# Kernel optimization log

Hardware: AMD Instinct MI355X
Metric: run time of the kernel (lower is better)

The kernel has to match this reference:

```python
import jax, jax.numpy as jnp
import numpy as np

N_NODES = 100000
N_EDGES = 1600000
N_FEAT = 128
N_HID = 128
N_CLS = 40
DROP_P = 0.5


def setup_inputs() -> dict:
    key = jax.random.key(0)
    k1, k2, k3, k4 = jax.random.split(key, 4)
    x = jax.random.normal(k1, (N_NODES, N_FEAT), dtype=jnp.float32)
    edge_index = jax.random.randint(k2, (2, N_EDGES), 0, N_NODES, dtype=jnp.int32)
    W1 = jax.random.normal(k3, (N_FEAT, N_HID), dtype=jnp.float32) / np.sqrt(N_FEAT)
    b1 = jnp.zeros((N_HID,), dtype=jnp.float32)
    W2 = jax.random.normal(k4, (N_HID, N_CLS), dtype=jnp.float32) / np.sqrt(N_HID)
    b2 = jnp.zeros((N_CLS,), dtype=jnp.float32)
    return {"x": x, "edge_index": edge_index, "W1": W1, "b1": b1, "W2": W2, "b2": b2}


def _gcn_norm(edge_index, num_nodes):
    # add self-loops, then symmetric normalization D^-1/2 (A+I) D^-1/2
    loops = jnp.arange(num_nodes, dtype=edge_index.dtype)
    src = jnp.concatenate([edge_index[0], loops])
    dst = jnp.concatenate([edge_index[1], loops])
    deg = jax.ops.segment_sum(jnp.ones_like(dst, dtype=jnp.float32), dst,
                              num_segments=num_nodes)
    deg_isqrt = jax.lax.rsqrt(deg)  # deg >= 1 thanks to self-loops
    norm = deg_isqrt[src] * deg_isqrt[dst]  # [E+N]
    return src, dst, norm


def _gcn_conv(x, src, dst, norm, W, b, num_nodes):
    h = x @ W                                   # [N, out]
    msg = h[src] * norm[:, None]                # gather + scale, [E+N, out]
    out = jax.ops.segment_sum(msg, dst, num_segments=num_nodes)  # scatter-add
    return out + b


def reference(x, edge_index, W1, b1, W2, b2):
    num_nodes = x.shape[0]
    src, dst, norm = _gcn_norm(edge_index, num_nodes)
    h = _gcn_conv(x, src, dst, norm, W1, b1, num_nodes)
    h = jax.nn.relu(h)
    # dropout(p=0.5, training=True) with a fixed key for determinism
    keep = jax.random.uniform(jax.random.key(42), h.shape) >= DROP_P
    h = jnp.where(keep, h / (1.0 - DROP_P), 0.0)
    out = _gcn_conv(h, src, dst, norm, W2, b2, num_nodes)
    return out
```

## Files before the change

### kernel.cpp

```cpp
#include <hip/hip_runtime.h>

#define N_NODES 100000
#define N_EDGES 1600000
#define NBUCK 196
#define G1B 1563
#define FB 391
#define FEDGE 4096
#define BCAP 9216

typedef __attribute__((ext_vector_type(8))) short short8v;
typedef __attribute__((ext_vector_type(4))) float f32x4;

__device__ __forceinline__ unsigned pack_bf16(float a, float b){
  unsigned ua = __float_as_uint(a), ub = __float_as_uint(b);
  ua = ua + 0x7fffu + ((ua >> 16) & 1u);
  ub = ub + 0x7fffu + ((ub >> 16) & 1u);
  return (ua >> 16) | (ub & 0xffff0000u);
}
__device__ __forceinline__ unsigned short bf16_of(float a){
  unsigned ua = __float_as_uint(a);
  ua = ua + 0x7fffu + ((ua >> 16) & 1u);
  return (unsigned short)(ua >> 16);
}
__device__ __forceinline__ float bf_lo(unsigned u){ return __uint_as_float(u << 16); }
__device__ __forceinline__ float bf_hi(unsigned u){ return __uint_as_float(u & 0xffff0000u); }

__device__ __forceinline__ unsigned tf_rotl(unsigned x, int r){ return (x<<r)|(x>>(32-r)); }

__device__ __forceinline__ unsigned dropout_keep(unsigned e){
  unsigned x0 = 0u, x1 = e;
  const unsigned k0 = 0u, k1v = 42u;
  const unsigned k2 = 0x1BD11BDAu ^ k0 ^ k1v;
#define TF_R(r) { x0 += x1; x1 = tf_rotl(x1,(r)); x1 ^= x0; }
  x0 += k0; x1 += k1v;
  TF_R(13) TF_R(15) TF_R(26) TF_R(6)
  x0 += k1v; x1 += k2 + 1u;
  TF_R(17) TF_R(29) TF_R(16) TF_R(24)
  x0 += k2; x1 += k0 + 2u;
  TF_R(13) TF_R(15) TF_R(26) TF_R(6)
  x0 += k0; x1 += k1v + 3u;
  TF_R(17) TF_R(29) TF_R(16) TF_R(24)
  x0 += k1v; x1 += k2 + 4u;
  TF_R(13) TF_R(15) TF_R(26) TF_R(6)
  x0 += k2; x1 += k0 + 5u;
#undef TF_R
  return (x0 ^ x1) >> 31;
}

__global__ void k_wt(const float* __restrict__ W1, unsigned short* __restrict__ W1T){
  int idx = blockIdx.x*256 + threadIdx.x;
  int k = idx >> 7, n = idx & 127;
  W1T[n*128 + k] = bf16_of(W1[idx]);
}

__launch_bounds__(256)
__global__ void k_B(const float* __restrict__ x, const unsigned short* __restrict__ W1T,
                    unsigned short* __restrict__ h1u,
                    const int* __restrict__ src, const int* __restrict__ dst,
                    int* __restrict__ bcur2, int2* __restrict__ tmp, int N, int E){
  __shared__ int hist[NBUCK];
  int t = threadIdx.x;
  if (blockIdx.x < FB){
    int fb = blockIdx.x;
    for (int i = t; i < NBUCK; i += 256) hist[i] = 0;
    __syncthreads();
    int e0 = fb*FEDGE;
    #pragma unroll 4
    for (int j = 0; j < FEDGE/256; j++){
      int e = e0 + t + j*256;
      if (e < E) atomicAdd(&hist[dst[e] >> 9], 1);
    }
    __syncthreads();
    if (t < NBUCK){
      int c = hist[t];
      if (c > 0) hist[t] = t*BCAP + atomicAdd(&bcur2[t], c);
    }
    __syncthreads();
    #pragma unroll 4
    for (int j = 0; j < FEDGE/256; j++){
      int e = e0 + t + j*256;
      if (e < E){
        int d = dst[e], s = src[e];
        int p = atomicAdd(&hist[d >> 9], 1);
        tmp[p] = make_int2(s, d);
      }
    }
    return;
  }
  int gb = blockIdx.x - FB;
  if (gb >= G1B) return;
  int w = t >> 6, l = t & 63;
  int lo = l & 15, hi = l >> 4;
  int rowA = gb*64 + w*16 + lo;
  int rA = (rowA < N) ? rowA : (N-1);
  const float4* xr = (const float4*)(x + (size_t)rA*128);

  short8v a[4];
  #pragma unroll
  for (int kk = 0; kk < 4; kk++){
    float4 f0 = xr[kk*8 + 2*hi];
    float4 f1 = xr[kk*8 + 2*hi + 1];
    union { short8v v; unsigned u[4]; } A;
    A.u[0] = pack_bf16(f0.x, f0.y);
    A.u[1] = pack_bf16(f0.z, f0.w);
    A.u[2] = pack_bf16(f1.x, f1.y);
    A.u[3] = pack_bf16(f1.z, f1.w);
    a[kk] = A.v;
  }
  int rowC0 = gb*64 + w*16 + hi*4;
  #pragma unroll
  for (int tt = 0; tt < 8; tt++){
    int n0 = tt*16;
    const uint4* brow = (const uint4*)(W1T + (n0 + lo)*128);
    f32x4 acc = {0.f, 0.f, 0.f, 0.f};
    #pragma unroll
    for (int kk = 0; kk < 4; kk++){
      union { short8v v; uint4 q; } B;
      B.q = brow[kk*4 + hi];
      acc = __builtin_amdgcn_mfma_f32_16x16x32_bf16(a[kk], B.v, acc, 0, 0, 0);
    }
    int colC = n0 + lo;
    #pragma unroll
    for (int r = 0; r < 4; r++){
      int rc = rowC0 + r;
      if (rc < N) h1u[(size_t)rc*128 + colC] = bf16_of(acc[r]);
    }
  }
}

__launch_bounds__(512)
__global__ void k_hist(const int2* __restrict__ tmp, const int* __restrict__ bcur2,
                       int* __restrict__ degi, int* __restrict__ off,
                       float* __restrict__ dii, int N){
  __shared__ int cur[512];
  __shared__ int wtot[8];
  int b = blockIdx.x, t = threadIdx.x;
  cur[t] = 0;
  __syncthreads();
  int m = bcur2[b];
  int base = b*BCAP;
  int node0 = b << 9;
  for (int i = t; i < m; i += 512)
    atomicAdd(&cur[tmp[base + i].y - node0], 1);
  __syncthreads();
  int v = cur[t];
  int lane = t & 63, w = t >> 6;
  int incl = v;
  for (int d = 1; d < 64; d <<= 1){
    int y = __shfl_up(incl, d);
    if (lane >= d) incl += y;
  }
  if (lane == 63) wtot[w] = incl;
  __syncthreads();
  int wb = 0;
  for (int i = 0; i < w; i++) wb += wtot[i];
  int excl = wb + incl - v;
  int n = node0 + t;
  if (n < N){
    degi[n] = v;
    off[n]  = base + excl;
    dii[n]  = rsqrtf((float)(v + 1));
  }
}

__launch_bounds__(1024)
__global__ void k_csort(const int2* __restrict__ tmp, int2* __restrict__ csre,
                        const int* __restrict__ off, const int* __restrict__ bcur2,
                        const float* __restrict__ dii, int N){
  __shared__ int   cur[512];
  __shared__ float dl[512];
  int b = blockIdx.x, t = threadIdx.x;
  int node0 = b << 9;
  if (t < 512){
    int n = node0 + t;
    cur[t] = (n < N) ? off[n] : 0;
    dl[t]  = (n < N) ? dii[n] : 0.f;
  }
  __syncthreads();
  int m = bcur2[b];
  int base = b*BCAP;
  for (int i = t; i < m; i += 1024){
    int2 r = tmp[base + i];
    int dloc = r.y - node0;
    float w = dii[r.x] * dl[dloc];
    int p = atomicAdd(&cur[dloc], 1);
    csre[p] = make_int2(r.x, __float_as_int(w));
  }
}

__launch_bounds__(256)
__global__ void k_agg1(const unsigned* __restrict__ h1g, unsigned* __restrict__ Bbg,
                       const int2* __restrict__ csre, const int* __restrict__ off,
                       const int* __restrict__ degi, const float* __restrict__ dii,
                       const float* __restrict__ b1, int N){
  int n = blockIdx.x*4 + (threadIdx.x >> 6);
  int lane = threadIdx.x & 63;
  if (n >= N) return;
  n = __builtin_amdgcn_readfirstlane(n);
  float din = dii[n];
  float s2 = din*din;
  unsigned su = h1g[(size_t)n*64 + lane];
  float a0 = bf_lo(su)*s2, a1 = bf_hi(su)*s2;
  int o = off[n], cnt = degi[n];
  int i = 0;
  for (; i + 8 <= cnt; i += 8){
    int2 e0 = csre[o+i+0], e1 = csre[o+i+1], e2 = csre[o+i+2], e3 = csre[o+i+3];
    int2 e4 = csre[o+i+4], e5 = csre[o+i+5], e6 = csre[o+i+6], e7 = csre[o+i+7];
    unsigned u0 = h1g[(size_t)e0.x*64 + lane];
    unsigned u1 = h1g[(size_t)e1.x*64 + lane];
    unsigned u2 = h1g[(size_t)e2.x*64 + lane];
    unsigned u3 = h1g[(size_t)e3.x*64 + lane];
    unsigned u4 = h1g[(size_t)e4.x*64 + lane];
    unsigned u5 = h1g[(size_t)e5.x*64 + lane];
    unsigned u6 = h1g[(size_t)e6.x*64 + lane];
    unsigned u7 = h1g[(size_t)e7.x*64 + lane];
    float w0 = __int_as_float(e0.y), w1 = __int_as_float(e1.y);
    float w2 = __int_as_float(e2.y), w3 = __int_as_float(e3.y);
    float w4 = __int_as_float(e4.y), w5 = __int_as_float(e5.y);
    float w6 = __int_as_float(e6.y), w7 = __int_as_float(e7.y);
    a0 = fmaf(bf_lo(u0), w0, a0); a1 = fmaf(bf_hi(u0), w0, a1);
    a0 = fmaf(bf_lo(u1), w1, a0); a1 = fmaf(bf_hi(u1), w1, a1);
    a0 = fmaf(bf_lo(u2), w2, a0); a1 = fmaf(bf_hi(u2), w2, a1);
    a0 = fmaf(bf_lo(u3), w3, a0); a1 = fmaf(bf_hi(u3), w3, a1);
    a0 = fmaf(bf_lo(u4), w4, a0); a1 = fmaf(bf_hi(u4), w4, a1);
    a0 = fmaf(bf_lo(u5), w5, a0); a1 = fmaf(bf_hi(u5), w5, a1);
    a0 = fmaf(bf_lo(u6), w6, a0); a1 = fmaf(bf_hi(u6), w6, a1);
    a0 = fmaf(bf_lo(u7), w7, a0); a1 = fmaf(bf_hi(u7), w7, a1);
  }
  for (; i < cnt; ++i){
    int2 e = csre[o+i];
    unsigned u = h1g[(size_t)e.x*64 + lane];
    float w = __int_as_float(e.y);
    a0 = fmaf(bf_lo(u), w, a0); a1 = fmaf(bf_hi(u), w, a1);
  }
  float2 bb = *(const float2*)(b1 + lane*2);
  a0 = fmaxf(a0 + bb.x, 0.f);
  a1 = fmaxf(a1 + bb.y, 0.f);
  unsigned e0i = (unsigned)n*128u + (unsigned)lane*2u;
  a0 = dropout_keep(e0i)      ? a0*2.f : 0.f;
  a1 = dropout_keep(e0i + 1u) ? a1*2.f : 0.f;
  Bbg[(size_t)n*64 + lane] = pack_bf16(a0, a1);
}

__launch_bounds__(256)
__global__ void k_gemm2(const unsigned* __restrict__ Bbg, const float* __restrict__ W2,
                        unsigned short* __restrict__ h2p, int N){
  __shared__ float W2T[40*132];
  __shared__ float Bs[64*132];
  int t = threadIdx.x;
  int row0 = blockIdx.x * 64;
  for (int idx = t; idx < 128*40; idx += 256){
    int r = idx / 40, c = idx - 40*r;
    W2T[c*132 + r] = W2[idx];
  }
  #pragma unroll
  for (int j = 0; j < 8; j++){
    int idx = t + 256*j;
    int r = idx >> 5, c2 = idx & 31;
    int gr = row0 + r; if (gr > N-1) gr = N-1;
    uint2 v = *(const uint2*)(Bbg + (size_t)gr*64 + c2*2);
    float4 f = { bf_lo(v.x), bf_hi(v.x), bf_lo(v.y), bf_hi(v.y) };
    *(float4*)(Bs + r*132 + c2*4) = f;
  }
  __syncthreads();

  int cg = t & 7, rg = t >> 3;
  int c0 = cg*5, r0 = rg*2;
  float acc[2][5] = {};
  #pragma unroll 4
  for (int k = 0; k < 128; k++){
    float bv0 = Bs[r0*132 + k], bv1 = Bs[(r0+1)*132 + k];
    #pragma unroll
    for (int u = 0; u < 5; u++){
      float w = W2T[(c0+u)*132 + k];
      acc[0][u] = fmaf(bv0, w, acc[0][u]);
      acc[1][u] = fmaf(bv1, w, acc[1][u]);
    }
  }
  #pragma unroll
  for (int i = 0; i < 2; i++){
    int gr = row0 + r0 + i;
    if (gr < N){
      #pragma unroll
      for (int u = 0; u < 5; u++) h2p[(size_t)gr*64 + c0 + u] = bf16_of(acc[i][u]);
    }
  }
}

__launch_bounds__(256)
__global__ void k_agg2(const unsigned* __restrict__ h2p, float* __restrict__ out,
                       const int2* __restrict__ csre, const int* __restrict__ off,
                       const int* __restrict__ degi, const float* __restrict__ dii,
                       const float* __restrict__ b2, int N){
  int n = blockIdx.x*4 + (threadIdx.x >> 6);
  int lane31 = threadIdx.x & 31;
  int lane   = threadIdx.x & 63;
  if (n >= N) return;
  n = __builtin_amdgcn_readfirstlane(n);
  float din = dii[n];
  float s2 = din*din;
  unsigned su = h2p[(size_t)n*32 + lane31];
  float a0 = bf_lo(su)*s2, a1 = bf_hi(su)*s2;
  int o = off[n], cnt = degi[n];
  int i = 0;
  for (; i + 8 <= cnt; i += 8){
    int2 e0 = csre[o+i+0], e1 = csre[o+i+1], e2 = csre[o+i+2], e3 = csre[o+i+3];
    int2 e4 = csre[o+i+4], e5 = csre[o+i+5], e6 = csre[o+i+6], e7 = csre[o+i+7];
    unsigned u0 = h2p[(size_t)e0.x*32 + lane31];
    unsigned u1 = h2p[(size_t)e1.x*32 + lane31];
    unsigned u2 = h2p[(size_t)e2.x*32 + lane31];
    unsigned u3 = h2p[(size_t)e3.x*32 + lane31];
    unsigned u4 = h2p[(size_t)e4.x*32 + lane31];
    unsigned u5 = h2p[(size_t)e5.x*32 + lane31];
    unsigned u6 = h2p[(size_t)e6.x*32 + lane31];
    unsigned u7 = h2p[(size_t)e7.x*32 + lane31];
    float w0 = __int_as_float(e0.y), w1 = __int_as_float(e1.y);
    float w2 = __int_as_float(e2.y), w3 = __int_as_float(e3.y);
    float w4 = __int_as_float(e4.y), w5 = __int_as_float(e5.y);
    float w6 = __int_as_float(e6.y), w7 = __int_as_float(e7.y);
    a0 = fmaf(bf_lo(u0), w0, a0); a1 = fmaf(bf_hi(u0), w0, a1);
    a0 = fmaf(bf_lo(u1), w1, a0); a1 = fmaf(bf_hi(u1), w1, a1);
    a0 = fmaf(bf_lo(u2), w2, a0); a1 = fmaf(bf_hi(u2), w2, a1);
    a0 = fmaf(bf_lo(u3), w3, a0); a1 = fmaf(bf_hi(u3), w3, a1);
    a0 = fmaf(bf_lo(u4), w4, a0); a1 = fmaf(bf_hi(u4), w4, a1);
    a0 = fmaf(bf_lo(u5), w5, a0); a1 = fmaf(bf_hi(u5), w5, a1);
    a0 = fmaf(bf_lo(u6), w6, a0); a1 = fmaf(bf_hi(u6), w6, a1);
    a0 = fmaf(bf_lo(u7), w7, a0); a1 = fmaf(bf_hi(u7), w7, a1);
  }
  for (; i < cnt; ++i){
    int2 e = csre[o+i];
    unsigned u = h2p[(size_t)e.x*32 + lane31];
    float w = __int_as_float(e.y);
    a0 = fmaf(bf_lo(u), w, a0); a1 = fmaf(bf_hi(u), w, a1);
  }
  if (lane < 20){
    float2 bb = *(const float2*)(b2 + lane*2);
    a0 += bb.x;
    a1 += bb.y;
    *(float2*)(out + (size_t)n*40 + lane*2) = make_float2(a0, a1);
  }
}

extern "C" void kernel_launch(void* const* d_in, const int* in_sizes, int n_in,
                              void* d_out, int out_size, void* d_ws, size_t ws_size,
                              hipStream_t stream){
  const float* x  = (const float*)d_in[0];
  const int*   ei = (const int*)  d_in[1];
  const float* W1 = (const float*)d_in[2];
  const float* b1 = (const float*)d_in[3];
  const float* W2 = (const float*)d_in[4];
  const float* b2 = (const float*)d_in[5];
  float* out = (float*)d_out;
  char* ws = (char*)d_ws;
  const int N = N_NODES, E = N_EDGES;
  const int* srcv = ei;
  const int* dstv = ei + E;

  int*   bcur2 = (int*)  (ws + 0);
  int*   off   = (int*)  (ws + 8192);
  int*   degi  = (int*)  (ws + 417792);
  float* dii   = (float*)(ws + 827392);
  unsigned short* W1T = (unsigned short*)(ws + 1236992);
  int2*  tmp   = (int2*) (ws + 1269760);
  int2*  csre  = (int2*) (ws + 15720448);
  unsigned short* h1u = (unsigned short*)(ws + 30171136);
  unsigned*       h1g = (unsigned*)      (ws + 30171136);
  unsigned short* h2p = (unsigned short*)(ws + 30171136);
  unsigned*       Bbg = (unsigned*)      (ws + 55771136);

  hipMemsetAsync(bcur2, 0, 8192, stream);
  k_wt<<<64, 256, 0, stream>>>(W1, W1T);

  k_B<<<FB + G1B, 256, 0, stream>>>(x, W1T, h1u, srcv, dstv, bcur2, tmp, N, E);
  k_hist<<<NBUCK, 512, 0, stream>>>(tmp, bcur2, degi, off, dii, N);
  k_csort<<<NBUCK, 1024, 0, stream>>>(tmp, csre, off, bcur2, dii, N);

  k_agg1 <<<N/4, 256, 0, stream>>>(h1g, Bbg, csre, off, degi, dii, b1, N);
  k_gemm2<<<(N + 63)/64, 256, 0, stream>>>(Bbg, W2, h2p, N);
  k_agg2 <<<N/4, 256, 0, stream>>>((const unsigned*)h2p, out, csre, off, degi, dii, b2, N);
}
```

Before: 229.7 us.

## Pack edges to 32 bits, merge sort kernels, use MFMA for second GEMM

Packs src and local dst into one 32-bit word and stores only the source index in the CSR, recomputing normalization weights from dii during aggregation. Merges the histogram and counting-sort kernels into one, folds the memset and weight transposes into a single init kernel, and replaces the scalar LDS-based second GEMM with bf16 MFMA using a padded transposed W2. This reduces edge-list bandwidth and launch count, at the cost of an extra dii gather per edge in both aggregation kernels.

```diff
diff --git a/kernel.cpp b/kernel.cpp
--- a/kernel.cpp
+++ b/kernel.cpp
@@ -47,17 +47,28 @@
   return (x0 ^ x1) >> 31;
 }
 
-__global__ void k_wt(const float* __restrict__ W1, unsigned short* __restrict__ W1T){
-  int idx = blockIdx.x*256 + threadIdx.x;
-  int k = idx >> 7, n = idx & 127;
-  W1T[n*128 + k] = bf16_of(W1[idx]);
+__global__ void k_init(const float* __restrict__ W1, const float* __restrict__ W2,
+                       unsigned short* __restrict__ W1T, unsigned short* __restrict__ W2T48,
+                       int* __restrict__ bcur2){
+  int b = blockIdx.x, t = threadIdx.x;
+  if (b < 64){
+    int idx = b*256 + t;
+    int k = idx >> 7, n = idx & 127;
+    W1T[n*128 + k] = bf16_of(W1[idx]);
+  } else {
+    if (t < NBUCK) bcur2[t] = 0;
+    for (int i = t; i < 48*128; i += 256){
+      int c = i >> 7, k = i & 127;
+      W2T48[c*128 + k] = (c < 40) ? bf16_of(W2[k*40 + c]) : (unsigned short)0;
+    }
+  }
 }
 
 __launch_bounds__(256)
 __global__ void k_B(const float* __restrict__ x, const unsigned short* __restrict__ W1T,
                     unsigned short* __restrict__ h1u,
                     const int* __restrict__ src, const int* __restrict__ dst,
-                    int* __restrict__ bcur2, int2* __restrict__ tmp, int N, int E){
+                    int* __restrict__ bcur2, unsigned* __restrict__ tmp, int N, int E){
   __shared__ int hist[NBUCK];
   int t = threadIdx.x;
   if (blockIdx.x < FB){
@@ -82,7 +93,7 @@
       if (e < E){
         int d = dst[e], s = src[e];
         int p = atomicAdd(&hist[d >> 9], 1);
-        tmp[p] = make_int2(s, d);
+        tmp[p] = ((unsigned)(d & 511) << 17) | (unsigned)s;
       }
     }
     return;
@@ -128,69 +139,58 @@
   }
 }
 
-__launch_bounds__(512)
-__global__ void k_hist(const int2* __restrict__ tmp, const int* __restrict__ bcur2,
+__launch_bounds__(1024)
+__global__ void k_sort(const unsigned* __restrict__ tmp, const int* __restrict__ bcur2,
                        int* __restrict__ degi, int* __restrict__ off,
-                       float* __restrict__ dii, int N){
+                       float* __restrict__ dii, unsigned* __restrict__ csr, int N){
   __shared__ int cur[512];
   __shared__ int wtot[8];
   int b = blockIdx.x, t = threadIdx.x;
-  cur[t] = 0;
+  if (t < 512) cur[t] = 0;
   __syncthreads();
   int m = bcur2[b];
   int base = b*BCAP;
   int node0 = b << 9;
-  for (int i = t; i < m; i += 512)
-    atomicAdd(&cur[tmp[base + i].y - node0], 1);
+  for (int i = t; i < m; i += 1024)
+    atomicAdd(&cur[tmp[base + i] >> 17], 1);
   __syncthreads();
-  int v = cur[t];
-  int lane = t & 63, w = t >> 6;
-  int incl = v;
-  for (int d = 1; d < 64; d <<= 1){
-    int y = __shfl_up(incl, d);
-    if (lane >= d) incl += y;
-  }
-  if (lane == 63) wtot[w] = incl;
+  int v = 0, excl = 0;
+  if (t < 512){
+    v = cur[t];
+    int lane = t & 63, w = t >> 6;
+    int incl = v;
+    for (int d = 1; d < 64; d <<= 1){
+      int y = __shfl_up(incl, d);
+      if (lane >= d) incl += y;
+    }
+    if (lane == 63) wtot[w] = incl;
+    __syncthreads();
+    int wb = 0;
+    for (int i = 0; i < w; i++) wb += wtot[i];
+    excl = wb + incl - v;
+    int n = node0 + t;
+    if (n < N){
+      degi[n] = v;
+      off[n]  = base + excl;
+      dii[n]  = rsqrtf((float)(v + 1));
+    }
+  } else {
+    __syncthreads();
+  }
   __syncthreads();
-  int wb = 0;
-  for (int i = 0; i < w; i++) wb += wtot[i];
-  int excl = wb + incl - v;
-  int n = node0 + t;
-  if (n < N){
-    degi[n] = v;
-    off[n]  = base + excl;
-    dii[n]  = rsqrtf((float)(v + 1));
-  }
-}
-
-__launch_bounds__(1024)
-__global__ void k_csort(const int2* __restrict__ tmp, int2* __restrict__ csre,
-                        const int* __restrict__ off, const int* __restrict__ bcur2,
-                        const float* __restrict__ dii, int N){
-  __shared__ int   cur[512];
-  __shared__ float dl[512];
-  int b = blockIdx.x, t = threadIdx.x;
-  int node0 = b << 9;
-  if (t < 512){
-    int n = node0 + t;
-    cur[t] = (n < N) ? off[n] : 0;
-    dl[t]  = (n < N) ? dii[n] : 0.f;
-  }
+  if (t < 512) cur[t] = base + excl;
   __syncthreads();
-  int m = bcur2[b];
-  int base = b*BCAP;
   for (int i = t; i < m; i += 1024){
-    int2 r = tmp[base + i];
-    int dloc = r.y - node0;
-    float w = dii[r.x] * dl[dloc];
+    unsigned e = tmp[base + i];
+    int dloc = e >> 17;
     int p = atomicAdd(&cur[dloc], 1);
-    csre[p] = make_int2(r.x, __float_as_int(w));
+    csr[p] = e & 0x1FFFFu;
   }
 }
 
 __launch_bounds__(256)
 __global__ void k_agg1(const unsigned* __restrict__ h1g, unsigned* __restrict__ Bbg,
-                       const int2* __restrict__ csre, const int* __restrict__ off,
+                       const unsigned* __restrict__ csr, const int* __restrict__ off,
                        const int* __restrict__ degi, const float* __restrict__ dii,
                        const float* __restrict__ b1, int N){
   int n = blockIdx.x*4 + (threadIdx.x >> 6);
@@ -204,20 +204,18 @@
   int o = off[n], cnt = degi[n];
   int i = 0;
   for (; i + 8 <= cnt; i += 8){
-    int2 e0 = csre[o+i+0], e1 = csre[o+i+1], e2 = csre[o+i+2], e3 = csre[o+i+3];
-    int2 e4 = csre[o+i+4], e5 = csre[o+i+5], e6 = csre[o+i+6], e7 = csre[o+i+7];
-    unsigned u0 = h1g[(size_t)e0.x*64 + lane];
-    unsigned u1 = h1g[(size_t)e1.x*64 + lane];
-    unsigned u2 = h1g[(size_t)e2.x*64 + lane];
-    unsigned u3 = h1g[(size_t)e3.x*64 + lane];
-    unsigned u4 = h1g[(size_t)e4.x*64 + lane];
-    unsigned u5 = h1g[(size_t)e5.x*64 + lane];
-    unsigned u6 = h1g[(size_t)e6.x*64 + lane];
-    unsigned u7 = h1g[(size_t)e7.x*64 + lane];
-    float w0 = __int_as_float(e0.y), w1 = __int_as_float(e1.y);
-    float w2 = __int_as_float(e2.y), w3 = __int_as_float(e3.y);
-    float w4 = __int_as_float(e4.y), w5 = __int_as_float(e5.y);
-    float w6 = __int_as_float(e6.y), w7 = __int_as_float(e7.y);
+    unsigned s0 = csr[o+i+0], s1 = csr[o+i+1], s2i = csr[o+i+2], s3 = csr[o+i+3];
+    unsigned s4 = csr[o+i+4], s5 = csr[o+i+5], s6 = csr[o+i+6], s7 = csr[o+i+7];
+    float w0 = dii[s0]*din, w1 = dii[s1]*din, w2 = dii[s2i]*din, w3 = dii[s3]*din;
+    float w4 = dii[s4]*din, w5 = dii[s5]*din, w6 = dii[s6]*din, w7 = dii[s7]*din;
+    unsigned u0 = h1g[(size_t)s0*64 + lane];
+    unsigned u1 = h1g[(size_t)s1*64 + lane];
+    unsigned u2 = h1g[(size_t)s2i*64 + lane];
+    unsigned u3 = h1g[(size_t)s3*64 + lane];
+    unsigned u4 = h1g[(size_t)s4*64 + lane];
+    unsigned u5 = h1g[(size_t)s5*64 + lane];
+    unsigned u6 = h1g[(size_t)s6*64 + lane];
+    unsigned u7 = h1g[(size_t)s7*64 + lane];
     a0 = fmaf(bf_lo(u0), w0, a0); a1 = fmaf(bf_hi(u0), w0, a1);
     a0 = fmaf(bf_lo(u1), w1, a0); a1 = fmaf(bf_hi(u1), w1, a1);
     a0 = fmaf(bf_lo(u2), w2, a0); a1 = fmaf(bf_hi(u2), w2, a1);
@@ -228,9 +226,9 @@
     a0 = fmaf(bf_lo(u7), w7, a0); a1 = fmaf(bf_hi(u7), w7, a1);
   }
   for (; i < cnt; ++i){
-    int2 e = csre[o+i];
-    unsigned u = h1g[(size_t)e.x*64 + lane];
-    float w = __int_as_float(e.y);
+    unsigned s = csr[o+i];
+    float w = dii[s]*din;
+    unsigned u = h1g[(size_t)s*64 + lane];
     a0 = fmaf(bf_lo(u), w, a0); a1 = fmaf(bf_hi(u), w, a1);
   }
   float2 bb = *(const float2*)(b1 + lane*2);
@@ -243,53 +241,46 @@
 }
 
 __launch_bounds__(256)
-__global__ void k_gemm2(const unsigned* __restrict__ Bbg, const float* __restrict__ W2,
+__global__ void k_gemm2(const unsigned* __restrict__ Bbg, const unsigned short* __restrict__ W2T48,
                         unsigned short* __restrict__ h2p, int N){
-  __shared__ float W2T[40*132];
-  __shared__ float Bs[64*132];
   int t = threadIdx.x;
-  int row0 = blockIdx.x * 64;
-  for (int idx = t; idx < 128*40; idx += 256){
-    int r = idx / 40, c = idx - 40*r;
-    W2T[c*132 + r] = W2[idx];
-  }
+  int w = t >> 6, l = t & 63;
+  int lo = l & 15, hi = l >> 4;
+  int rowA = blockIdx.x*64 + w*16 + lo;
+  int rA = (rowA < N) ? rowA : (N-1);
+  const uint4* ar = (const uint4*)(Bbg + (size_t)rA*64);
+
+  short8v a[4];
   #pragma unroll
-  for (int j = 0; j < 8; j++){
-    int idx = t + 256*j;
-    int r = idx >> 5, c2 = idx & 31;
-    int gr = row0 + r; if (gr > N-1) gr = N-1;
-    uint2 v = *(const uint2*)(Bbg + (size_t)gr*64 + c2*2);
-    float4 f = { bf_lo(v.x), bf_hi(v.x), bf_lo(v.y), bf_hi(v.y) };
-    *(float4*)(Bs + r*132 + c2*4) = f;
-  }
-  __syncthreads();
-
-  int cg = t & 7, rg = t >> 3;
-  int c0 = cg*5, r0 = rg*2;
-  float acc[2][5] = {};
-  #pragma unroll 4
-  for (int k = 0; k < 128; k++){
-    float bv0 = Bs[r0*132 + k], bv1 = Bs[(r0+1)*132 + k];
+  for (int kk = 0; kk < 4; kk++){
+    union { short8v v; uint4 q; } A;
+    A.q = ar[kk*4 + hi];
+    a[kk] = A.v;
+  }
+  int rowC0 = blockIdx.x*64 + w*16 + hi*4;
+  #pragma unroll
+  for (int tt = 0; tt < 3; tt++){
+    int n0 = tt*16;
+    const uint4* brow = (const uint4*)(W2T48 + (n0 + lo)*128);
+    f32x4 acc = {0.f, 0.f, 0.f, 0.f};
     #pragma unroll
-    for (int u = 0; u < 5; u++){
-      float w = W2T[(c0+u)*132 + k];
-      acc[0][u] = fmaf(bv0, w, acc[0][u]);
-      acc[1][u] = fmaf(bv1, w, acc[1][u]);
-    }
-  }
-  #pragma unroll
-  for (int i = 0; i < 2; i++){
-    int gr = row0 + r0 + i;
-    if (gr < N){
-      #pragma unroll
-      for (int u = 0; u < 5; u++) h2p[(size_t)gr*64 + c0 + u] = bf16_of(acc[i][u]);
+    for (int kk = 0; kk < 4; kk++){
+      union { short8v v; uint4 q; } B;
+      B.q = brow[kk*4 + hi];
+      acc = __builtin_amdgcn_mfma_f32_16x16x32_bf16(a[kk], B.v, acc, 0, 0, 0);
+    }
+    int colC = n0 + lo;
+    #pragma unroll
+    for (int r = 0; r < 4; r++){
+      int rc = rowC0 + r;
+      if (rc < N) h2p[(size_t)rc*64 + colC] = bf16_of(acc[r]);
     }
   }
 }
 
 __launch_bounds__(256)
 __global__ void k_agg2(const unsigned* __restrict__ h2p, float* __restrict__ out,
-                       const int2* __restrict__ csre, const int* __restrict__ off,
+                       const unsigned* __restrict__ csr, const int* __restrict__ off,
                        const int* __restrict__ degi, const float* __restrict__ dii,
                        const float* __restrict__ b2, int N){
   int n = blockIdx.x*4 + (threadIdx.x >> 6);
@@ -298,26 +289,24 @@
   if (n >= N) return;
   n = __builtin_amdgcn_readfirstlane(n);
   float din = dii[n];
-  float s2 = din*din;
+  float sq = din*din;
   unsigned su = h2p[(size_t)n*32 + lane31];
-  float a0 = bf_lo(su)*s2, a1 = bf_hi(su)*s2;
+  float a0 = bf_lo(su)*sq, a1 = bf_hi(su)*sq;
   int o = off[n], cnt = degi[n];
   int i = 0;
   for (; i + 8 <= cnt; i += 8){
-    int2 e0 = csre[o+i+0], e1 = csre[o+i+1], e2 = csre[o+i+2], e3 = csre[o+i+3];
-    int2 e4 = csre[o+i+4], e5 = csre[o+i+5], e6 = csre[o+i+6], e7 = csre[o+i+7];
-    unsigned u0 = h2p[(size_t)e0.x*32 + lane31];
-    unsigned u1 = h2p[(size_t)e1.x*32 + lane31];
-    unsigned u2 = h2p[(size_t)e2.x*32 + lane31];
-    unsigned u3 = h2p[(size_t)e3.x*32 + lane31];
-    unsigned u4 = h2p[(size_t)e4.x*32 + lane31];
-    unsigned u5 = h2p[(size_t)e5.x*32 + lane31];
-    unsigned u6 = h2p[(size_t)e6.x*32 + lane31];
-    unsigned u7 = h2p[(size_t)e7.x*32 + lane31];
-    float w0 = __int_as_float(e0.y), w1 = __int_as_float(e1.y);
-    float w2 = __int_as_float(e2.y), w3 = __int_as_float(e3.y);
-    float w4 = __int_as_float(e4.y), w5 = __int_as_float(e5.y);
-    float w6 = __int_as_float(e6.y), w7 = __int_as_float(e7.y);
+    unsigned s0 = csr[o+i+0], s1 = csr[o+i+1], s2i = csr[o+i+2], s3 = csr[o+i+3];
+    unsigned s4 = csr[o+i+4], s5 = csr[o+i+5], s6 = csr[o+i+6], s7 = csr[o+i+7];
+    float w0 = dii[s0]*din, w1 = dii[s1]*din, w2 = dii[s2i]*din, w3 = dii[s3]*din;
+    float w4 = dii[s4]*din, w5 = dii[s5]*din, w6 = dii[s6]*din, w7 = dii[s7]*din;
+    unsigned u0 = h2p[(size_t)s0*32 + lane31];
+    unsigned u1 = h2p[(size_t)s1*32 + lane31];
+    unsigned u2 = h2p[(size_t)s2i*32 + lane31];
+    unsigned u3 = h2p[(size_t)s3*32 + lane31];
+    unsigned u4 = h2p[(size_t)s4*32 + lane31];
+    unsigned u5 = h2p[(size_t)s5*32 + lane31];
+    unsigned u6 = h2p[(size_t)s6*32 + lane31];
+    unsigned u7 = h2p[(size_t)s7*32 + lane31];
     a0 = fmaf(bf_lo(u0), w0, a0); a1 = fmaf(bf_hi(u0), w0, a1);
     a0 = fmaf(bf_lo(u1), w1, a0); a1 = fmaf(bf_hi(u1), w1, a1);
     a0 = fmaf(bf_lo(u2), w2, a0); a1 = fmaf(bf_hi(u2), w2, a1);
@@ -328,9 +317,9 @@
     a0 = fmaf(bf_lo(u7), w7, a0); a1 = fmaf(bf_hi(u7), w7, a1);
   }
   for (; i < cnt; ++i){
-    int2 e = csre[o+i];
-    unsigned u = h2p[(size_t)e.x*32 + lane31];
-    float w = __int_as_float(e.y);
+    unsigned s = csr[o+i];
+    float w = dii[s]*din;
+    unsigned u = h2p[(size_t)s*32 + lane31];
     a0 = fmaf(bf_lo(u), w, a0); a1 = fmaf(bf_hi(u), w, a1);
   }
   if (lane < 20){
@@ -360,22 +349,20 @@
   int*   off   = (int*)  (ws + 8192);
   int*   degi  = (int*)  (ws + 417792);
   float* dii   = (float*)(ws + 827392);
-  unsigned short* W1T = (unsigned short*)(ws + 1236992);
-  int2*  tmp   = (int2*) (ws + 1269760);
-  int2*  csre  = (int2*) (ws + 15720448);
-  unsigned short* h1u = (unsigned short*)(ws + 30171136);
-  unsigned*       h1g = (unsigned*)      (ws + 30171136);
-  unsigned short* h2p = (unsigned short*)(ws + 30171136);
-  unsigned*       Bbg = (unsigned*)      (ws + 55771136);
-
-  hipMemsetAsync(bcur2, 0, 8192, stream);
-  k_wt<<<64, 256, 0, stream>>>(W1, W1T);
-
+  unsigned short* W1T   = (unsigned short*)(ws + 1236992);
+  unsigned short* W2T48 = (unsigned short*)(ws + 1269760);
+  unsigned* tmp = (unsigned*)(ws + 1290240);
+  unsigned* csr = (unsigned*)(ws + 8519680);
+  unsigned short* h1u = (unsigned short*)(ws + 16777216);
+  unsigned*       h1g = (unsigned*)      (ws + 16777216);
+  unsigned short* h2p = (unsigned short*)(ws + 16777216);
+  unsigned*       Bbg = (unsigned*)      (ws + 50331648);
+
+  k_init<<<65, 256, 0, stream>>>(W1, W2, W1T, W2T48, bcur2);
   k_B<<<FB + G1B, 256, 0, stream>>>(x, W1T, h1u, srcv, dstv, bcur2, tmp, N, E);
-  k_hist<<<NBUCK, 512, 0, stream>>>(tmp, bcur2, degi, off, dii, N);
-  k_csort<<<NBUCK, 1024, 0, stream>>>(tmp, csre, off, bcur2, dii, N);
-
-  k_agg1 <<<N/4, 256, 0, stream>>>(h1g, Bbg, csre, off, degi, dii, b1, N);
-  k_gemm2<<<(N + 63)/64, 256, 0, stream>>>(Bbg, W2, h2p, N);
-  k_agg2 <<<N/4, 256, 0, stream>>>((const unsigned*)h2p, out, csre, off, degi, dii, b2, N);
-}
+  k_sort<<<NBUCK, 1024, 0, stream>>>(tmp, bcur2, degi, off, dii, csr, N);
+
+  k_agg1 <<<N/4, 256, 0, stream>>>(h1g, Bbg, csr, off, degi, dii, b1, N);
+  k_gemm2<<<(N + 63)/64, 256, 0, stream>>>(Bbg, W2T48, h2p, N);
+  k_agg2 <<<N/4, 256, 0, stream>>>((const unsigned*)h2p, out, csr, off, degi, dii, b2, N);
+}
```

After: 216.0 us. 6.0% less time.
